# Optimization experiments

Measured on AMD Instinct MI355X. Metric: run time of the kernel, lower is better.

Reference implementation:

```python
import jax, jax.numpy as jnp
import numpy as np
import math


def proxy_delta_linear(x, W, gain):
    # x: [B,T,Din], W: [Dout,Din], gain: [1,1,Dout]
    D = x.shape[-1]
    xa = jnp.tanh(x)
    wa = jnp.tanh(W)
    x_sq = jnp.sum(xa * xa, axis=-1, keepdims=True)          # [B,T,1]
    w_sq = jnp.sum(wa * wa, axis=-1)                          # [Dout]
    dot = jnp.einsum('btd,od->bto', xa, wa)                   # [B,T,Dout]
    l2_sq = jnp.clip(x_sq + w_sq - 2.0 * dot, 0.0)
    out = 1.0 - l2_sq / D
    return (out - 0.5) * gain


def setup_inputs() -> dict:
    key = jax.random.key(0)
    ks = jax.random.split(key, 6)
    B, T, C = 2, 2048, 1024
    return {
        'x':  jax.random.normal(ks[0], (B, T, C), dtype=jnp.float32),
        'Wq': jax.random.normal(ks[1], (C, C), dtype=jnp.float32) * 0.02,
        'gq': jnp.full((1, 1, C), 2.0, dtype=jnp.float32),
        'Wk': jax.random.normal(ks[2], (C, C), dtype=jnp.float32) * 0.02,
        'gk': jnp.full((1, 1, C), 2.0, dtype=jnp.float32),
        'Wv': jax.random.normal(ks[3], (C, C), dtype=jnp.float32) * 0.02,
        'gv': jnp.full((1, 1, C), 2.0, dtype=jnp.float32),
        'Wo': jax.random.normal(ks[4], (C, C), dtype=jnp.float32) * 0.02,
    }


def reference(x, Wq, gq, Wk, gk, Wv, gv, Wo):
    B, T, C = x.shape
    H = 16
    D = C // H
    scale = math.sqrt(D)
    q = jnp.tanh(proxy_delta_linear(x, Wq, gq)).reshape(B, T, H, D).transpose(0, 2, 1, 3)
    k = jnp.tanh(proxy_delta_linear(x, Wk, gk)).reshape(B, T, H, D).transpose(0, 2, 1, 3)
    v = proxy_delta_linear(x, Wv, gv).reshape(B, T, H, D).transpose(0, 2, 1, 3)
    q_sq = jnp.sum(q * q, axis=-1, keepdims=True)             # [B,H,T,1]
    k_sq = jnp.sum(k * k, axis=-1)[:, :, None, :]             # [B,H,1,T]
    dot = jnp.einsum('bhtd,bhsd->bhts', q, k)                 # [B,H,T,T]
    dist_sq = jnp.clip(q_sq + k_sq - 2.0 * dot, 0.0)
    logits = -dist_sq / (scale * 10.0)
    attn = jax.nn.softmax(logits, axis=-1)
    out = jnp.einsum('bhts,bhsd->bhtd', attn, v)
    out = out.transpose(0, 2, 1, 3).reshape(B, T, C)
    return jnp.einsum('btc,oc->bto', out, Wo)
```

## Files before the change

kernel.cpp:

```cpp
#include <hip/hip_runtime.h>
#include <hip/hip_bf16.h>
#include <math.h>

typedef unsigned short u16;
typedef unsigned int u32;
typedef __attribute__((ext_vector_type(8))) short short8;
typedef __attribute__((ext_vector_type(8))) unsigned short ushort8;
typedef __attribute__((ext_vector_type(4))) float floatx4;
typedef __attribute__((ext_vector_type(16))) float floatx16;
typedef __attribute__((ext_vector_type(4))) u32 uint4v;

#define CDIM   1024
#define TSEQ   2048
#define NHEAD  16
#define HDIM   64

#define C2_CONST  (-0.01803368801111874f)
#define M2C2_CONST (0.03606737602223748f)

static __device__ __forceinline__ u16 f2bf(float f) {
    u32 u = __float_as_uint(f);
    u += 0x7fffu + ((u >> 16) & 1u);
    return (u16)(u >> 16);
}

static __device__ __forceinline__ u32 cvtpk(float a, float b) {
    u32 r;
    asm("v_cvt_pk_bf16_f32 %0, %1, %2" : "=v"(r) : "v"(a), "v"(b));
    return r;
}

static __device__ __forceinline__ float ftanh(float x) {
    float e = exp2f(x * 2.88539008f);
    float r = __builtin_amdgcn_rcpf(e + 1.0f);
    return fmaf(-2.0f, r, 1.0f);
}

static __device__ __forceinline__ void gll16(const void* g, void* l) {
    __builtin_amdgcn_global_load_lds(
        (const __attribute__((address_space(1))) unsigned int*)g,
        (__attribute__((address_space(3))) unsigned int*)l, 16, 0, 0);
}

__global__ __launch_bounds__(256) void prep(const float* __restrict__ x,
                                            const float* __restrict__ Wq, const float* __restrict__ Wk,
                                            const float* __restrict__ Wv, const float* __restrict__ Wo,
                                            u16* __restrict__ xa,
                                            u16* __restrict__ waq, u16* __restrict__ wak,
                                            u16* __restrict__ wav, u16* __restrict__ wob,
                                            float* __restrict__ xsq,
                                            float* __restrict__ sqq, float* __restrict__ sqk,
                                            float* __restrict__ sqv) {
    __shared__ float red[4];
    int bid = blockIdx.x, tid = threadIdx.x;
    const float* src; u16* dst; float* sq; int row; bool do_tanh = true;
    if (bid < 4096) {
        row = bid; src = x; dst = xa; sq = xsq;
    } else {
        int mat = (bid - 4096) >> 10; row = (bid - 4096) & 1023;
        src = (mat == 0) ? Wq : (mat == 1) ? Wk : (mat == 2) ? Wv : Wo;
        dst = (mat == 0) ? waq : (mat == 1) ? wak : (mat == 2) ? wav : wob;
        sq  = (mat == 0) ? sqq : (mat == 1) ? sqk : (mat == 2) ? sqv : nullptr;
        do_tanh = (mat < 3);
    }
    float4 v = reinterpret_cast<const float4*>(src + (size_t)row * CDIM)[tid];
    if (do_tanh) {
        float a0 = ftanh(v.x), a1 = ftanh(v.y), a2 = ftanh(v.z), a3 = ftanh(v.w);
        *reinterpret_cast<ushort4*>(dst + (size_t)row * CDIM + tid * 4) =
            make_ushort4(f2bf(a0), f2bf(a1), f2bf(a2), f2bf(a3));
        float s = a0*a0 + a1*a1 + a2*a2 + a3*a3;
        #pragma unroll
        for (int m = 1; m < 64; m <<= 1) s += __shfl_xor(s, m, 64);
        if ((tid & 63) == 0) red[tid >> 6] = s;
        __syncthreads();
        if (tid == 0 && sq) sq[row] = red[0] + red[1] + red[2] + red[3];
    } else {
        *reinterpret_cast<ushort4*>(dst + (size_t)row * CDIM + tid * 4) =
            make_ushort4(f2bf(v.x), f2bf(v.y), f2bf(v.z), f2bf(v.w));
    }
}

__global__ __launch_bounds__(256) void gemm_qkv(const u16* __restrict__ xa,
                                                const u16* __restrict__ waq, const u16* __restrict__ wak, const u16* __restrict__ wav,
                                                u16* __restrict__ qb, u16* __restrict__ kb, u16* __restrict__ vT,
                                                const float* __restrict__ xsq,
                                                const float* __restrict__ sqq, const float* __restrict__ sqk, const float* __restrict__ sqv,
                                                const float* __restrict__ gq, const float* __restrict__ gk, const float* __restrict__ gv,
                                                float* __restrict__ ksC2T) {
    __shared__ __align__(16) u16 As[128 * 64];
    __shared__ __align__(16) u16 Bs[128 * 64];
    int z = blockIdx.z;
    const u16* Bm     = (z == 0) ? waq : (z == 1) ? wak : wav;
    const float* wsq  = (z == 0) ? sqq : (z == 1) ? sqk : sqv;
    const float* gain = (z == 0) ? gq : (z == 1) ? gk : gv;

    int tid = threadIdx.x;
    int m0 = blockIdx.y * 128, n0 = blockIdx.x * 128;
    int w = tid >> 6, l = tid & 63, wm = w >> 1, wn = w & 1, g = l >> 4, c = l & 15;
    int r8 = l >> 3, sl7 = l & 7;
    int cmask = (c & 7) ^ (c >> 3);

    floatx4 acc[4][4] = {};

    for (int kt = 0; kt < 16; ++kt) {
        __syncthreads();
        #pragma unroll
        for (int i = 0; i < 4; i++) {
            int ch = w * 4 + i;
            int row = ch * 8 + r8;
            int sl = sl7 ^ r8 ^ (ch & 1);
            gll16(xa + (size_t)(m0 + row) * CDIM + kt * 64 + sl * 8, &As[ch * 512 + l * 8]);
            gll16(Bm + (size_t)(n0 + row) * CDIM + kt * 64 + sl * 8, &Bs[ch * 512 + l * 8]);
        }
        __syncthreads();
        short8 af[2][4], bf[2][4];
        #pragma unroll
        for (int kk = 0; kk < 2; kk++) {
            #pragma unroll
            for (int mi = 0; mi < 4; mi++)
                af[kk][mi] = *reinterpret_cast<const short8*>(
                    &As[(wm * 64 + mi * 16 + c) * 64 + (((kk * 4 + g) ^ cmask) << 3)]);
            #pragma unroll
            for (int ni = 0; ni < 4; ni++)
                bf[kk][ni] = *reinterpret_cast<const short8*>(
                    &Bs[(wn * 64 + ni * 16 + c) * 64 + (((kk * 4 + g) ^ cmask) << 3)]);
        }
        #pragma unroll
        for (int kk = 0; kk < 2; kk++)
            #pragma unroll
            for (int mi = 0; mi < 4; mi++)
                #pragma unroll
                for (int ni = 0; ni < 4; ni++)
                    acc[mi][ni] = __builtin_amdgcn_mfma_f32_16x16x32_bf16(af[kk][mi], bf[kk][ni], acc[mi][ni], 0, 0, 0);
    }

    if (z < 2) {
        u16* outH = (z == 0) ? qb : kb;
        float part[4][4] = {};
        #pragma unroll
        for (int mi = 0; mi < 4; mi++) {
            int rowb = m0 + wm * 64 + mi * 16 + g * 4;
            #pragma unroll
            for (int ni = 0; ni < 4; ni++) {
                int col = n0 + wn * 64 + ni * 16 + c;
                float wsqc = wsq[col], gn = gain[col];
                #pragma unroll
                for (int r = 0; r < 4; r++) {
                    float l2 = fmaxf(xsq[rowb + r] + wsqc - 2.f * acc[mi][ni][r], 0.f);
                    float th = ftanh((0.5f - l2 * (1.f / 1024.f)) * gn);
                    outH[(size_t)(rowb + r) * CDIM + col] = f2bf(th);
                    part[mi][r] += th * th;
                }
            }
        }
        if (z == 1) {
            int hh = blockIdx.x * 2 + wn;
            #pragma unroll
            for (int mi = 0; mi < 4; mi++)
                #pragma unroll
                for (int r = 0; r < 4; r++) {
                    float s = part[mi][r];
                    s += __shfl_xor(s, 1, 64); s += __shfl_xor(s, 2, 64);
                    s += __shfl_xor(s, 4, 64); s += __shfl_xor(s, 8, 64);
                    if (c == 0) {
                        int row = m0 + wm * 64 + mi * 16 + g * 4 + r;
                        int bb = row >> 11, t = row & 2047;
                        ksC2T[(size_t)(bb * NHEAD + hh) * TSEQ + t] = s * C2_CONST;
                    }
                }
        }
    } else {
        #pragma unroll
        for (int mi = 0; mi < 4; mi++) {
            int rowb = m0 + wm * 64 + mi * 16 + g * 4;
            #pragma unroll
            for (int ni = 0; ni < 4; ni++) {
                int col = n0 + wn * 64 + ni * 16 + c;
                float wsqc = wsq[col], gn = gain[col];
                float vals[4];
                #pragma unroll
                for (int r = 0; r < 4; r++) {
                    float l2 = fmaxf(xsq[rowb + r] + wsqc - 2.f * acc[mi][ni][r], 0.f);
                    vals[r] = (0.5f - l2 * (1.f / 1024.f)) * gn;
                }
                int bb = rowb >> 11, t0 = rowb & 2047;
                int hh = col >> 6, dd = col & 63;
                ushort4 pv = make_ushort4(f2bf(vals[0]), f2bf(vals[1]), f2bf(vals[2]), f2bf(vals[3]));
                *reinterpret_cast<ushort4*>(&vT[(((size_t)(bb * NHEAD + hh) * HDIM + dd) << 11) + t0]) = pv;
            }
        }
    }
}

__global__ __launch_bounds__(256) void gemm_out(const u16* __restrict__ A, const u16* __restrict__ Bm,
                                                float* __restrict__ outF) {
    __shared__ __align__(16) u16 As[128 * 64];
    __shared__ __align__(16) u16 Bs[128 * 64];
    int tid = threadIdx.x;
    int m0 = blockIdx.y * 128, n0 = blockIdx.x * 128;
    int w = tid >> 6, l = tid & 63, wm = w >> 1, wn = w & 1, g = l >> 4, c = l & 15;
    int r8 = l >> 3, sl7 = l & 7;
    int cmask = (c & 7) ^ (c >> 3);

    floatx4 acc[4][4] = {};

    for (int kt = 0; kt < 16; ++kt) {
        __syncthreads();
        #pragma unroll
        for (int i = 0; i < 4; i++) {
            int ch = w * 4 + i;
            int row = ch * 8 + r8;
            int sl = sl7 ^ r8 ^ (ch & 1);
            gll16(A + (size_t)(m0 + row) * CDIM + kt * 64 + sl * 8, &As[ch * 512 + l * 8]);
            gll16(Bm + (size_t)(n0 + row) * CDIM + kt * 64 + sl * 8, &Bs[ch * 512 + l * 8]);
        }
        __syncthreads();
        short8 af[2][4], bf[2][4];
        #pragma unroll
        for (int kk = 0; kk < 2; kk++) {
            #pragma unroll
            for (int mi = 0; mi < 4; mi++)
                af[kk][mi] = *reinterpret_cast<const short8*>(
                    &As[(wm * 64 + mi * 16 + c) * 64 + (((kk * 4 + g) ^ cmask) << 3)]);
            #pragma unroll
            for (int ni = 0; ni < 4; ni++)
                bf[kk][ni] = *reinterpret_cast<const short8*>(
                    &Bs[(wn * 64 + ni * 16 + c) * 64 + (((kk * 4 + g) ^ cmask) << 3)]);
        }
        #pragma unroll
        for (int kk = 0; kk < 2; kk++)
            #pragma unroll
            for (int mi = 0; mi < 4; mi++)
                #pragma unroll
                for (int ni = 0; ni < 4; ni++)
                    acc[mi][ni] = __builtin_amdgcn_mfma_f32_16x16x32_bf16(af[kk][mi], bf[kk][ni], acc[mi][ni], 0, 0, 0);
    }

    #pragma unroll
    for (int mi = 0; mi < 4; mi++) {
        int rowb = m0 + wm * 64 + mi * 16 + g * 4;
        #pragma unroll
        for (int ni = 0; ni < 4; ni++) {
            int col = n0 + wn * 64 + ni * 16 + c;
            #pragma unroll
            for (int r = 0; r < 4; r++)
                outF[(size_t)(rowb + r) * CDIM + col] = acc[mi][ni][r];
        }
    }
}

__global__ __launch_bounds__(256, 2) void attn6(const u16* __restrict__ q, const u16* __restrict__ k,
                                                const u16* __restrict__ vT,
                                                const float* __restrict__ ksC2T, u16* __restrict__ ao) {
    int tt = blockIdx.x, h = blockIdx.y, b = blockIdx.z;
    int tid = threadIdx.x, w = tid >> 6, l = tid & 63;
    int hi = l >> 5, t32 = l & 31;
    int twb = tt * 128 + w * 32;

    __shared__ __align__(16) u16 Ks[2][64 * 64];
    __shared__ __align__(16) u16 Vs[2][64 * 64];
    __shared__ __align__(16) float Ls[4][32];

    short8 qf[4];
    size_t qrow = (size_t)(b * TSEQ + twb + t32) * CDIM + h * HDIM;
    #pragma unroll
    for (int ks = 0; ks < 4; ks++)
        qf[ks] = *reinterpret_cast<const short8*>(&q[qrow + ks * 16 + hi * 8]);

    const float* ksb = ksC2T + (size_t)(b * NHEAD + h) * TSEQ;
    const u16* kbase = k + (size_t)(b * TSEQ) * CDIM + h * HDIM;
    const u16* vbase = vT + (size_t)(b * NHEAD + h) * HDIM * TSEQ;

    int r8 = l >> 3, sl7 = l & 7;
    int lmask = (l & 7) ^ ((l >> 3) & 1);

    floatx16 oacc[2] = {};
    float lrun = 0.f;

    #pragma unroll
    for (int i = 0; i < 2; i++) {
        int ch = w * 2 + i;
        int sl = sl7 ^ r8 ^ (ch & 1);
        gll16(kbase + (size_t)(ch * 8 + r8) * CDIM + sl * 8, &Ks[0][ch * 512 + l * 8]);
        gll16(vbase + (size_t)(ch * 8 + r8) * TSEQ + sl * 8, &Vs[0][ch * 512 + l * 8]);
    }
    __syncthreads();

    for (int st = 0; st < 32; ++st) {
        int cur = st & 1;
        if (st < 31) {
            int s1 = (st + 1) * 64;
            #pragma unroll
            for (int i = 0; i < 2; i++) {
                int ch = w * 2 + i;
                int sl = sl7 ^ r8 ^ (ch & 1);
                gll16(kbase + (size_t)(s1 + ch * 8 + r8) * CDIM + sl * 8, &Ks[cur ^ 1][ch * 512 + l * 8]);
                gll16(vbase + (size_t)(ch * 8 + r8) * TSEQ + s1 + sl * 8, &Vs[cur ^ 1][ch * 512 + l * 8]);
            }
        }

        #pragma unroll
        for (int stile = 0; stile < 2; ++stile) {
            floatx16 sxx = {};
            #pragma unroll
            for (int kstep = 0; kstep < 4; kstep++) {
                int row = stile * 32 + t32;
                int slot = (kstep * 2 + hi) ^ lmask;
                short8 kf = *reinterpret_cast<const short8*>(&Ks[cur][row * 64 + slot * 8]);
                sxx = __builtin_amdgcn_mfma_f32_32x32x16_bf16(kf, qf[kstep], sxx, 0, 0, 0);
            }

            u32 pk[8];
            #pragma unroll
            for (int qq = 0; qq < 4; qq++) {
                float4 kc = *reinterpret_cast<const float4*>(
                    &ksb[st * 64 + stile * 32 + qq * 8 + hi * 4]);
                float p0 = exp2f(fmaf(sxx[qq * 4 + 0], M2C2_CONST, kc.x));
                float p1 = exp2f(fmaf(sxx[qq * 4 + 1], M2C2_CONST, kc.y));
                float p2 = exp2f(fmaf(sxx[qq * 4 + 2], M2C2_CONST, kc.z));
                float p3 = exp2f(fmaf(sxx[qq * 4 + 3], M2C2_CONST, kc.w));
                lrun += (p0 + p1) + (p2 + p3);
                pk[qq * 2]     = cvtpk(p0, p1);
                pk[qq * 2 + 1] = cvtpk(p2, p3);
            }

            u32 ex[4];
            #pragma unroll
            for (int m = 0; m < 4; m++) {
                const int p0a[4] = {0, 1, 4, 5};
                u32 send = hi ? pk[p0a[m]] : pk[p0a[m] + 2];
                ex[m] = (u32)__shfl_xor((int)send, 32, 64);
            }

            #pragma unroll
            for (int e = 0; e < 2; e++) {
                int ks = stile * 2 + e;
                uint4v au;
                au.x = hi ? ex[2 * e]     : pk[4 * e];
                au.y = hi ? ex[2 * e + 1] : pk[4 * e + 1];
                au.z = hi ? pk[4 * e + 2] : ex[2 * e];
                au.w = hi ? pk[4 * e + 3] : ex[2 * e + 1];
                short8 af = __builtin_bit_cast(short8, au);
                #pragma unroll
                for (int dt = 0; dt < 2; dt++) {
                    int row = dt * 32 + t32;
                    int slot = (ks * 2 + hi) ^ lmask;
                    short8 vf = *reinterpret_cast<const short8*>(&Vs[cur][row * 64 + slot * 8]);
                    oacc[dt] = __builtin_amdgcn_mfma_f32_32x32x16_bf16(af, vf, oacc[dt], 0, 0, 0);
                }
            }
        }

        __syncthreads();
    }

    float ltot = lrun + __shfl_xor(lrun, 32, 64);
    if (l < 32) Ls[w][l] = ltot;
    float4 lv[4];
    #pragma unroll
    for (int qq = 0; qq < 4; qq++)
        lv[qq] = *reinterpret_cast<const float4*>(&Ls[w][qq * 8 + hi * 4]);
    #pragma unroll
    for (int dt = 0; dt < 2; dt++)
        #pragma unroll
        for (int r = 0; r < 16; ++r) {
            int trow = (r & 3) + 8 * (r >> 2) + 4 * hi;
            float lval = (r & 3) == 0 ? lv[r >> 2].x : (r & 3) == 1 ? lv[r >> 2].y
                       : (r & 3) == 2 ? lv[r >> 2].z : lv[r >> 2].w;
            ao[(size_t)(b * TSEQ + twb + trow) * CDIM + h * HDIM + dt * 32 + t32] =
                f2bf(oacc[dt][r] * __builtin_amdgcn_rcpf(lval));
        }
}

extern "C" void kernel_launch(void* const* d_in, const int* in_sizes, int n_in,
                              void* d_out, int out_size, void* d_ws, size_t ws_size,
                              hipStream_t stream) {
    const float* x  = (const float*)d_in[0];
    const float* Wq = (const float*)d_in[1];
    const float* gq = (const float*)d_in[2];
    const float* Wk = (const float*)d_in[3];
    const float* gk = (const float*)d_in[4];
    const float* Wv = (const float*)d_in[5];
    const float* gv = (const float*)d_in[6];
    const float* Wo = (const float*)d_in[7];
    float* out = (float*)d_out;

    char* p = (char*)d_ws;
    u16* xa  = (u16*)p;  p += (size_t)8 << 20;
    u16* qb  = (u16*)p;  p += (size_t)8 << 20;
    u16* kb  = (u16*)p;  p += (size_t)8 << 20;
    u16* vT  = (u16*)p;  p += (size_t)8 << 20;
    u16* ao  = (u16*)p;  p += (size_t)8 << 20;
    u16* waq = (u16*)p;  p += (size_t)2 << 20;
    u16* wak = (u16*)p;  p += (size_t)2 << 20;
    u16* wav = (u16*)p;  p += (size_t)2 << 20;
    u16* wob = (u16*)p;  p += (size_t)2 << 20;
    float* xsq   = (float*)p; p += 4096 * 4;
    float* sqq   = (float*)p; p += 1024 * 4;
    float* sqk   = (float*)p; p += 1024 * 4;
    float* sqv   = (float*)p; p += 1024 * 4;
    float* ksC2T = (float*)p; p += 4096 * 16 * 4;
    (void)ws_size; (void)in_sizes; (void)n_in; (void)out_size;

    prep<<<8192, 256, 0, stream>>>(x, Wq, Wk, Wv, Wo, xa, waq, wak, wav, wob,
                                   xsq, sqq, sqk, sqv);

    dim3 gqkv(8, 32, 3);
    gemm_qkv<<<gqkv, 256, 0, stream>>>(xa, waq, wak, wav, qb, kb, vT, xsq,
                                       sqq, sqk, sqv, gq, gk, gv, ksC2T);

    dim3 ga(16, NHEAD, 2);
    attn6<<<ga, 256, 0, stream>>>(qb, kb, vT, ksC2T, ao);

    dim3 gg(8, 32);
    gemm_out<<<gg, 256, 0, stream>>>(ao, wob, out);
}
```

Before: 162.4 us.

## Store Q/K/V in MFMA fragment order and split attention keys across waves

The QKV GEMM epilogue now writes Q, K and V directly in the per-lane MFMA fragment layout, so the attention kernel loads operands straight from global memory into registers with coalesced short8 loads, with no LDS staging or syncs. The attention kernel now uses 64-query blocks (1024 blocks), with two wave pairs each covering half the keys, and merges their partial outputs and row sums through shared memory. Occupancy hint is raised to 4 blocks per CU. The cost is scattered 2-byte stores in the Q/K epilogue, more global/L2 traffic since K/V are no longer shared via LDS across the four query waves, and an extra reduction step.

```diff
diff --git a/kernel.cpp b/kernel.cpp
--- a/kernel.cpp
+++ b/kernel.cpp
@@ -82,7 +82,7 @@
 
 __global__ __launch_bounds__(256) void gemm_qkv(const u16* __restrict__ xa,
                                                 const u16* __restrict__ waq, const u16* __restrict__ wak, const u16* __restrict__ wav,
-                                                u16* __restrict__ qb, u16* __restrict__ kb, u16* __restrict__ vT,
+                                                u16* __restrict__ qF, u16* __restrict__ kF, u16* __restrict__ vF,
                                                 const float* __restrict__ xsq,
                                                 const float* __restrict__ sqq, const float* __restrict__ sqk, const float* __restrict__ sqv,
                                                 const float* __restrict__ gq, const float* __restrict__ gk, const float* __restrict__ gv,
@@ -135,20 +135,25 @@
     }
 
     if (z < 2) {
-        u16* outH = (z == 0) ? qb : kb;
+        u16* outF = (z == 0) ? qF : kF;
         float part[4][4] = {};
         #pragma unroll
         for (int mi = 0; mi < 4; mi++) {
             int rowb = m0 + wm * 64 + mi * 16 + g * 4;
+            int bb = rowb >> 11, tt = rowb & 2047;
+            int tile = tt >> 5, l31 = tt & 31;
             #pragma unroll
             for (int ni = 0; ni < 4; ni++) {
                 int col = n0 + wn * 64 + ni * 16 + c;
+                int hh = col >> 6, d = col & 63;
+                int kst = d >> 4, hi8 = (d >> 3) & 1, j = d & 7;
+                size_t base = ((((size_t)(bb * NHEAD + hh) * 64 + tile) * 4 + kst) * 2 + hi8) * 256 + j;
                 float wsqc = wsq[col], gn = gain[col];
                 #pragma unroll
                 for (int r = 0; r < 4; r++) {
                     float l2 = fmaxf(xsq[rowb + r] + wsqc - 2.f * acc[mi][ni][r], 0.f);
                     float th = ftanh((0.5f - l2 * (1.f / 1024.f)) * gn);
-                    outH[(size_t)(rowb + r) * CDIM + col] = f2bf(th);
+                    outF[base + (size_t)(l31 + r) * 8] = f2bf(th);
                     part[mi][r] += th * th;
                 }
             }
@@ -173,9 +178,13 @@
         #pragma unroll
         for (int mi = 0; mi < 4; mi++) {
             int rowb = m0 + wm * 64 + mi * 16 + g * 4;
+            int bb = rowb >> 11, s = rowb & 2047;
+            int tile = s >> 5, e = (s >> 4) & 1, hi8 = (s >> 3) & 1, j0 = s & 7;
             #pragma unroll
             for (int ni = 0; ni < 4; ni++) {
                 int col = n0 + wn * 64 + ni * 16 + c;
+                int hh = col >> 6, d = col & 63;
+                int dt = d >> 5, l31 = d & 31;
                 float wsqc = wsq[col], gn = gain[col];
                 float vals[4];
                 #pragma unroll
@@ -183,10 +192,10 @@
                     float l2 = fmaxf(xsq[rowb + r] + wsqc - 2.f * acc[mi][ni][r], 0.f);
                     vals[r] = (0.5f - l2 * (1.f / 1024.f)) * gn;
                 }
-                int bb = rowb >> 11, t0 = rowb & 2047;
-                int hh = col >> 6, dd = col & 63;
-                ushort4 pv = make_ushort4(f2bf(vals[0]), f2bf(vals[1]), f2bf(vals[2]), f2bf(vals[3]));
-                *reinterpret_cast<ushort4*>(&vT[(((size_t)(bb * NHEAD + hh) * HDIM + dd) << 11) + t0]) = pv;
+                size_t idx = (((((size_t)(bb * NHEAD + hh) * 2 + dt) * 64 + tile) * 2 + e) * 2 + hi8) * 256
+                             + (size_t)l31 * 8 + j0;
+                *reinterpret_cast<ushort4*>(&vF[idx]) =
+                    make_ushort4(f2bf(vals[0]), f2bf(vals[1]), f2bf(vals[2]), f2bf(vals[3]));
             }
         }
     }
@@ -249,127 +258,115 @@
     }
 }
 
-__global__ __launch_bounds__(256, 2) void attn6(const u16* __restrict__ q, const u16* __restrict__ k,
-                                                const u16* __restrict__ vT,
+__global__ __launch_bounds__(256, 4) void attn7(const u16* __restrict__ qF, const u16* __restrict__ kF,
+                                                const u16* __restrict__ vF,
                                                 const float* __restrict__ ksC2T, u16* __restrict__ ao) {
-    int tt = blockIdx.x, h = blockIdx.y, b = blockIdx.z;
+    int bid = blockIdx.x;
+    int hb = bid & 31;
+    int ttile = bid >> 5;
     int tid = threadIdx.x, w = tid >> 6, l = tid & 63;
+    int qg = w >> 1, sc = w & 1;
     int hi = l >> 5, t32 = l & 31;
-    int twb = tt * 128 + w * 32;
-
-    __shared__ __align__(16) u16 Ks[2][64 * 64];
-    __shared__ __align__(16) u16 Vs[2][64 * 64];
-    __shared__ __align__(16) float Ls[4][32];
-
+
+    __shared__ float redO[2][64][33];
+    __shared__ float Ls[2][32];
+
+    const u16* qbase = qF + ((size_t)hb * 64 + ttile * 2 + qg) * 2048;
     short8 qf[4];
-    size_t qrow = (size_t)(b * TSEQ + twb + t32) * CDIM + h * HDIM;
     #pragma unroll
     for (int ks = 0; ks < 4; ks++)
-        qf[ks] = *reinterpret_cast<const short8*>(&q[qrow + ks * 16 + hi * 8]);
-
-    const float* ksb = ksC2T + (size_t)(b * NHEAD + h) * TSEQ;
-    const u16* kbase = k + (size_t)(b * TSEQ) * CDIM + h * HDIM;
-    const u16* vbase = vT + (size_t)(b * NHEAD + h) * HDIM * TSEQ;
-
-    int r8 = l >> 3, sl7 = l & 7;
-    int lmask = (l & 7) ^ ((l >> 3) & 1);
+        qf[ks] = *reinterpret_cast<const short8*>(qbase + ks * 512 + (size_t)l * 8);
+
+    const u16* kbase = kF + (size_t)hb * (64 * 2048);
+    const u16* vbase = vF + (size_t)hb * (2 * 64 * 1024);
+    const float* ksb = ksC2T + (size_t)hb * TSEQ;
 
     floatx16 oacc[2] = {};
     float lrun = 0.f;
 
-    #pragma unroll
-    for (int i = 0; i < 2; i++) {
-        int ch = w * 2 + i;
-        int sl = sl7 ^ r8 ^ (ch & 1);
-        gll16(kbase + (size_t)(ch * 8 + r8) * CDIM + sl * 8, &Ks[0][ch * 512 + l * 8]);
-        gll16(vbase + (size_t)(ch * 8 + r8) * TSEQ + sl * 8, &Vs[0][ch * 512 + l * 8]);
+    int st0 = sc * 32;
+    for (int st = st0; st < st0 + 32; ++st) {
+        const short8* kp = reinterpret_cast<const short8*>(kbase + (size_t)st * 2048) + l;
+        short8 kf0 = kp[0], kf1 = kp[64], kf2 = kp[128], kf3 = kp[192];
+        const short8* vp = reinterpret_cast<const short8*>(vbase + (size_t)st * 1024) + l;
+        short8 vf00 = vp[0], vf01 = vp[64];
+        short8 vf10 = vp[8192], vf11 = vp[8256];
+
+        floatx16 sxx = {};
+        sxx = __builtin_amdgcn_mfma_f32_32x32x16_bf16(kf0, qf[0], sxx, 0, 0, 0);
+        sxx = __builtin_amdgcn_mfma_f32_32x32x16_bf16(kf1, qf[1], sxx, 0, 0, 0);
+        sxx = __builtin_amdgcn_mfma_f32_32x32x16_bf16(kf2, qf[2], sxx, 0, 0, 0);
+        sxx = __builtin_amdgcn_mfma_f32_32x32x16_bf16(kf3, qf[3], sxx, 0, 0, 0);
+
+        u32 pk[8];
+        #pragma unroll
+        for (int qq = 0; qq < 4; qq++) {
+            float4 kc = *reinterpret_cast<const float4*>(&ksb[st * 32 + qq * 8 + hi * 4]);
+            float p0 = exp2f(fmaf(sxx[qq * 4 + 0], M2C2_CONST, kc.x));
+            float p1 = exp2f(fmaf(sxx[qq * 4 + 1], M2C2_CONST, kc.y));
+            float p2 = exp2f(fmaf(sxx[qq * 4 + 2], M2C2_CONST, kc.z));
+            float p3 = exp2f(fmaf(sxx[qq * 4 + 3], M2C2_CONST, kc.w));
+            lrun += (p0 + p1) + (p2 + p3);
+            pk[qq * 2]     = cvtpk(p0, p1);
+            pk[qq * 2 + 1] = cvtpk(p2, p3);
+        }
+
+        u32 ex[4];
+        #pragma unroll
+        for (int m = 0; m < 4; m++) {
+            const int p0a[4] = {0, 1, 4, 5};
+            u32 send = hi ? pk[p0a[m]] : pk[p0a[m] + 2];
+            ex[m] = (u32)__shfl_xor((int)send, 32, 64);
+        }
+
+        #pragma unroll
+        for (int e = 0; e < 2; e++) {
+            uint4v au;
+            au.x = hi ? ex[2 * e]     : pk[4 * e];
+            au.y = hi ? ex[2 * e + 1] : pk[4 * e + 1];
+            au.z = hi ? pk[4 * e + 2] : ex[2 * e];
+            au.w = hi ? pk[4 * e + 3] : ex[2 * e + 1];
+            short8 af = __builtin_bit_cast(short8, au);
+            oacc[0] = __builtin_amdgcn_mfma_f32_32x32x16_bf16(af, e ? vf01 : vf00, oacc[0], 0, 0, 0);
+            oacc[1] = __builtin_amdgcn_mfma_f32_32x32x16_bf16(af, e ? vf11 : vf10, oacc[1], 0, 0, 0);
+        }
+    }
+
+    if (sc == 1) {
+        #pragma unroll
+        for (int dt = 0; dt < 2; dt++)
+            #pragma unroll
+            for (int r = 0; r < 16; r++)
+                redO[qg][l][dt * 16 + r] = oacc[dt][r];
+        redO[qg][l][32] = lrun;
     }
     __syncthreads();
-
-    for (int st = 0; st < 32; ++st) {
-        int cur = st & 1;
-        if (st < 31) {
-            int s1 = (st + 1) * 64;
-            #pragma unroll
-            for (int i = 0; i < 2; i++) {
-                int ch = w * 2 + i;
-                int sl = sl7 ^ r8 ^ (ch & 1);
-                gll16(kbase + (size_t)(s1 + ch * 8 + r8) * CDIM + sl * 8, &Ks[cur ^ 1][ch * 512 + l * 8]);
-                gll16(vbase + (size_t)(ch * 8 + r8) * TSEQ + s1 + sl * 8, &Vs[cur ^ 1][ch * 512 + l * 8]);
+    if (sc == 0) {
+        #pragma unroll
+        for (int dt = 0; dt < 2; dt++)
+            #pragma unroll
+            for (int r = 0; r < 16; r++)
+                oacc[dt][r] += redO[qg][l][dt * 16 + r];
+        lrun += redO[qg][l][32];
+        float ltot = lrun + __shfl_xor(lrun, 32, 64);
+        if (l < 32) Ls[qg][l] = ltot;
+        int b = hb >> 4, h = hb & 15;
+        int twb = ttile * 64 + qg * 32;
+        float4 lv[4];
+        #pragma unroll
+        for (int qq = 0; qq < 4; qq++)
+            lv[qq] = *reinterpret_cast<const float4*>(&Ls[qg][qq * 8 + hi * 4]);
+        #pragma unroll
+        for (int dt = 0; dt < 2; dt++)
+            #pragma unroll
+            for (int r = 0; r < 16; ++r) {
+                int trow = (r & 3) + 8 * (r >> 2) + 4 * hi;
+                float lval = (r & 3) == 0 ? lv[r >> 2].x : (r & 3) == 1 ? lv[r >> 2].y
+                           : (r & 3) == 2 ? lv[r >> 2].z : lv[r >> 2].w;
+                ao[(size_t)(b * TSEQ + twb + trow) * CDIM + h * HDIM + dt * 32 + t32] =
+                    f2bf(oacc[dt][r] * __builtin_amdgcn_rcpf(lval));
             }
-        }
-
-        #pragma unroll
-        for (int stile = 0; stile < 2; ++stile) {
-            floatx16 sxx = {};
-            #pragma unroll
-            for (int kstep = 0; kstep < 4; kstep++) {
-                int row = stile * 32 + t32;
-                int slot = (kstep * 2 + hi) ^ lmask;
-                short8 kf = *reinterpret_cast<const short8*>(&Ks[cur][row * 64 + slot * 8]);
-                sxx = __builtin_amdgcn_mfma_f32_32x32x16_bf16(kf, qf[kstep], sxx, 0, 0, 0);
-            }
-
-            u32 pk[8];
-            #pragma unroll
-            for (int qq = 0; qq < 4; qq++) {
-                float4 kc = *reinterpret_cast<const float4*>(
-                    &ksb[st * 64 + stile * 32 + qq * 8 + hi * 4]);
-                float p0 = exp2f(fmaf(sxx[qq * 4 + 0], M2C2_CONST, kc.x));
-                float p1 = exp2f(fmaf(sxx[qq * 4 + 1], M2C2_CONST, kc.y));
-                float p2 = exp2f(fmaf(sxx[qq * 4 + 2], M2C2_CONST, kc.z));
-                float p3 = exp2f(fmaf(sxx[qq * 4 + 3], M2C2_CONST, kc.w));
-                lrun += (p0 + p1) + (p2 + p3);
-                pk[qq * 2]     = cvtpk(p0, p1);
-                pk[qq * 2 + 1] = cvtpk(p2, p3);
-            }
-
-            u32 ex[4];
-            #pragma unroll
-            for (int m = 0; m < 4; m++) {
-                const int p0a[4] = {0, 1, 4, 5};
-                u32 send = hi ? pk[p0a[m]] : pk[p0a[m] + 2];
-                ex[m] = (u32)__shfl_xor((int)send, 32, 64);
-            }
-
-            #pragma unroll
-            for (int e = 0; e < 2; e++) {
-                int ks = stile * 2 + e;
-                uint4v au;
-                au.x = hi ? ex[2 * e]     : pk[4 * e];
-                au.y = hi ? ex[2 * e + 1] : pk[4 * e + 1];
-                au.z = hi ? pk[4 * e + 2] : ex[2 * e];
-                au.w = hi ? pk[4 * e + 3] : ex[2 * e + 1];
-                short8 af = __builtin_bit_cast(short8, au);
-                #pragma unroll
-                for (int dt = 0; dt < 2; dt++) {
-                    int row = dt * 32 + t32;
-                    int slot = (ks * 2 + hi) ^ lmask;
-                    short8 vf = *reinterpret_cast<const short8*>(&Vs[cur][row * 64 + slot * 8]);
-                    oacc[dt] = __builtin_amdgcn_mfma_f32_32x32x16_bf16(af, vf, oacc[dt], 0, 0, 0);
-                }
-            }
-        }
-
-        __syncthreads();
-    }
-
-    float ltot = lrun + __shfl_xor(lrun, 32, 64);
-    if (l < 32) Ls[w][l] = ltot;
-    float4 lv[4];
-    #pragma unroll
-    for (int qq = 0; qq < 4; qq++)
-        lv[qq] = *reinterpret_cast<const float4*>(&Ls[w][qq * 8 + hi * 4]);
-    #pragma unroll
-    for (int dt = 0; dt < 2; dt++)
-        #pragma unroll
-        for (int r = 0; r < 16; ++r) {
-            int trow = (r & 3) + 8 * (r >> 2) + 4 * hi;
-            float lval = (r & 3) == 0 ? lv[r >> 2].x : (r & 3) == 1 ? lv[r >> 2].y
-                       : (r & 3) == 2 ? lv[r >> 2].z : lv[r >> 2].w;
-            ao[(size_t)(b * TSEQ + twb + trow) * CDIM + h * HDIM + dt * 32 + t32] =
-                f2bf(oacc[dt][r] * __builtin_amdgcn_rcpf(lval));
-        }
+    }
 }
 
 extern "C" void kernel_launch(void* const* d_in, const int* in_sizes, int n_in,
@@ -387,9 +384,9 @@
 
     char* p = (char*)d_ws;
     u16* xa  = (u16*)p;  p += (size_t)8 << 20;
-    u16* qb  = (u16*)p;  p += (size_t)8 << 20;
-    u16* kb  = (u16*)p;  p += (size_t)8 << 20;
-    u16* vT  = (u16*)p;  p += (size_t)8 << 20;
+    u16* qF  = (u16*)p;  p += (size_t)8 << 20;
+    u16* kF  = (u16*)p;  p += (size_t)8 << 20;
+    u16* vF  = (u16*)p;  p += (size_t)8 << 20;
     u16* ao  = (u16*)p;  p += (size_t)8 << 20;
     u16* waq = (u16*)p;  p += (size_t)2 << 20;
     u16* wak = (u16*)p;  p += (size_t)2 << 20;
@@ -406,11 +403,10 @@
                                    xsq, sqq, sqk, sqv);
 
     dim3 gqkv(8, 32, 3);
-    gemm_qkv<<<gqkv, 256, 0, stream>>>(xa, waq, wak, wav, qb, kb, vT, xsq,
+    gemm_qkv<<<gqkv, 256, 0, stream>>>(xa, waq, wak, wav, qF, kF, vF, xsq,
                                        sqq, sqk, sqv, gq, gk, gv, ksC2T);
 
-    dim3 ga(16, NHEAD, 2);
-    attn6<<<ga, 256, 0, stream>>>(qb, kb, vT, ksC2T, ao);
+    attn7<<<1024, 256, 0, stream>>>(qF, kF, vF, ksC2T, ao);
 
     dim3 gg(8, 32);
     gemm_out<<<gg, 256, 0, stream>>>(ao, wob, out);
```

Result: faster. 140.4 us (-13.5%).
